# Performance work log

Hardware: AMD Instinct MI355X
Metric: run time of the kernel (lower is better)

## Reference

```python
import jax, jax.numpy as jnp
import numpy as np

B, N, E, F, D = 8, 2000, 64000, 1024, 128
NEG_SLOPE = 0.01  # torch LeakyReLU default

def leaky(x):
    return jnp.where(x >= 0, x, NEG_SLOPE * x)

def gcn_conv(x, ei, W, b):
    # PyG GCNConv: add self loops, symmetric norm, x @ W, scatter-sum, + bias
    src, tgt = ei[0], ei[1]
    loops = jnp.arange(N, dtype=src.dtype)
    src_a = jnp.concatenate([src, loops])
    tgt_a = jnp.concatenate([tgt, loops])
    deg = jax.ops.segment_sum(jnp.ones(src_a.shape, x.dtype), tgt_a, num_segments=N)
    dinv = jnp.where(deg > 0, jax.lax.rsqrt(deg), 0.0)
    norm = dinv[src_a] * dinv[tgt_a]  # [E+N]
    h = x @ W                          # [N, F]
    out = jax.ops.segment_sum(norm[:, None] * h[src_a], tgt_a, num_segments=N)
    return out + b

gcn_conv_b = jax.vmap(gcn_conv, in_axes=(0, 0, None, None))

def setup_inputs() -> dict:
    key = jax.random.key(0)
    ks = jax.random.split(key, 16)
    s = lambda fan: 1.0 / np.sqrt(fan)
    return {
        "x1": jax.random.normal(ks[0], (B, N, F), jnp.float32),
        "ei1": jax.random.randint(ks[1], (B, 2, E), 0, N, jnp.int32),
        "x2": jax.random.normal(ks[2], (B, N, F), jnp.float32),
        "ei2": jax.random.randint(ks[3], (B, 2, E), 0, N, jnp.int32),
        "Wg1": jax.random.normal(ks[4], (F, F), jnp.float32) * s(F),
        "bg1": jnp.zeros((F,), jnp.float32),
        "Wf1": jax.random.normal(ks[5], (F, D), jnp.float32) * s(F),
        "bf1": jnp.zeros((D,), jnp.float32),
        "Wg2": jax.random.normal(ks[6], (F, F), jnp.float32) * s(F),
        "bg2": jnp.zeros((F,), jnp.float32),
        "Wf2": jax.random.normal(ks[7], (F, D), jnp.float32) * s(F),
        "bf2": jnp.zeros((D,), jnp.float32),
        "W1": jax.random.normal(ks[8], (2 * D, 256), jnp.float32) * s(2 * D),
        "b1": jnp.zeros((256,), jnp.float32),
        "W2": jax.random.normal(ks[9], (256, 64), jnp.float32) * s(256),
        "b2": jnp.zeros((64,), jnp.float32),
        "Wo": jax.random.normal(ks[10], (64, 1), jnp.float32) * s(64),
        "bo": jnp.zeros((1,), jnp.float32),
    }

def reference(x1, ei1, x2, ei2, Wg1, bg1, Wf1, bf1, Wg2, bg2, Wf2, bf2,
              W1, b1, W2, b2, Wo, bo):
    # branch 1
    h1 = leaky(gcn_conv_b(x1, ei1, Wg1, bg1))       # [B, N, F]
    g1 = jnp.mean(h1, axis=1)                        # [B, F]
    g1 = leaky(g1 @ Wf1 + bf1)                       # [B, D] (dropout = eval identity)
    # branch 2
    h2 = leaky(gcn_conv_b(x2, ei2, Wg2, bg2))
    g2 = jnp.mean(h2, axis=1)
    g2 = leaky(g2 @ Wf2 + bf2)
    # head
    xc = jnp.concatenate([g1, g2], axis=1)           # [B, 2D]
    xc = leaky(xc @ W1 + b1)
    xc = leaky(xc @ W2 + b2)
    return jax.nn.sigmoid(xc @ Wo + bo)              # [B, 1]
```

## Files before the change

### kernel.cpp

```cpp
#include <hip/hip_runtime.h>
#include <stdint.h>

#define B 8
#define NN 2000
#define EG 64000
#define FF 1024
#define DD 128
#define BK 32
#define NCHUNK 125
#define CG 5

#define NB_CONV 32000
#define NB_WT   2048
#define NB_DEG  4000
#define NB_GEMM 2048
#define NB_FILL 4000

typedef short short8 __attribute__((ext_vector_type(8)));
typedef float f32x4 __attribute__((ext_vector_type(4)));
typedef float f32x2 __attribute__((ext_vector_type(2)));

__device__ __forceinline__ unsigned short f2bf(float f) {
    union { float f; unsigned int u; } v; v.f = f;
    unsigned int u = v.u;
    unsigned int r = u + 0x7FFFu + ((u >> 16) & 1u);
    return (unsigned short)(r >> 16);
}
__device__ __forceinline__ float leaky(float v) { return v >= 0.0f ? v : 0.01f * v; }

__device__ __forceinline__ void acc8p(f32x2* __restrict__ r, float w, uint4 v) {
    union { unsigned int u; float f; } c;
    f32x2 wv = {w, w};
    f32x2 h;
    c.u = v.x << 16;          h.x = c.f;
    c.u = v.x & 0xffff0000u;  h.y = c.f;
    r[0] += wv * h;
    c.u = v.y << 16;          h.x = c.f;
    c.u = v.y & 0xffff0000u;  h.y = c.f;
    r[1] += wv * h;
    c.u = v.z << 16;          h.x = c.f;
    c.u = v.z & 0xffff0000u;  h.y = c.f;
    r[2] += wv * h;
    c.u = v.w << 16;          h.x = c.f;
    c.u = v.w & 0xffff0000u;  h.y = c.f;
    r[3] += wv * h;
}

__global__ void k_prep(const float* __restrict__ x_a, const float* __restrict__ x_b,
                       unsigned short* __restrict__ xb,
                       const float* __restrict__ Wg_a, const float* __restrict__ Wg_b,
                       unsigned short* __restrict__ wT,
                       const int* __restrict__ ei_a, const int* __restrict__ ei_b,
                       int* __restrict__ degi) {
    int blk = blockIdx.x;
    int tid = threadIdx.x;
    __shared__ float tile[32][33];
    if (blk < NB_CONV) {
        int i = blk * 256 + tid;
        float4 v = (i < NB_CONV * 128) ? ((const float4*)x_a)[i]
                                       : ((const float4*)x_b)[i - NB_CONV * 128];
        ushort4 o;
        o.x = f2bf(v.x); o.y = f2bf(v.y); o.z = f2bf(v.z); o.w = f2bf(v.w);
        ((ushort4*)xb)[i] = o;
    } else if (blk < NB_CONV + NB_WT) {
        int b2 = blk - NB_CONV;
        int z = b2 >> 10, rem = b2 & 1023;
        int by = rem >> 5, bx = rem & 31;
        int tx = tid & 31, ty = tid >> 5;
        int k0 = by * 32, n0 = bx * 32;
        const float* Wg = z ? Wg_b : Wg_a;
        unsigned short* o = wT + (size_t)z * FF * FF;
#pragma unroll
        for (int r = 0; r < 4; ++r) {
            int row = ty + r * 8;
            tile[row][tx] = Wg[(k0 + row) * FF + n0 + tx];
        }
        __syncthreads();
#pragma unroll
        for (int r = 0; r < 4; ++r) {
            int row = ty + r * 8;
            o[(n0 + row) * FF + k0 + tx] = f2bf(tile[tx][row]);
        }
    } else {
        int i = (blk - NB_CONV - NB_WT) * 256 + tid;
        int g = i / EG, e = i - g * EG;
        const int* ei = (g < B) ? (ei_a + (size_t)g * 2 * EG)
                                : (ei_b + (size_t)(g - B) * 2 * EG);
        int t = ei[EG + e];
        atomicAdd(&degi[g * NN + t], 1);
    }
}

__global__ void k_scan(const int* __restrict__ degi, int* __restrict__ csr_off,
                       int* __restrict__ cursor, float* __restrict__ dinv) {
    int g = blockIdx.x, t = threadIdx.x;
    __shared__ int part[256];
    int loc[8];
    int s = 0;
#pragma unroll
    for (int i = 0; i < 8; ++i) {
        int n = t * 8 + i;
        int c = (n < NN) ? degi[g * NN + n] : 0;
        if (n < NN) dinv[g * NN + n] = rsqrtf((float)(c + 1));
        loc[i] = s;
        s += c;
    }
    part[t] = s;
    __syncthreads();
    for (int off = 1; off < 256; off <<= 1) {
        int v = (t >= off) ? part[t - off] : 0;
        __syncthreads();
        part[t] += v;
        __syncthreads();
    }
    int base = part[t] - s;
#pragma unroll
    for (int i = 0; i < 8; ++i) {
        int n = t * 8 + i;
        if (n < NN) {
            int o = base + loc[i];
            csr_off[g * (NN + 1) + n] = o;
            cursor[g * NN + n] = o;
        }
    }
    if (t == 255) csr_off[g * (NN + 1) + NN] = part[255];
}

__launch_bounds__(256) __global__
void k_gemm_fill(const unsigned short* __restrict__ Abf, const unsigned short* __restrict__ wT,
                 unsigned short* __restrict__ Hbf,
                 const int* __restrict__ ei_a, const int* __restrict__ ei_b,
                 int* __restrict__ cursor, const float* __restrict__ dinv,
                 int2* __restrict__ epk) {
    int blk = blockIdx.x;
    __shared__ __align__(16) unsigned short As[128 * BK];
    __shared__ __align__(16) unsigned short Bs[128 * BK];
    if (blk >= NB_GEMM) {
        int i = (blk - NB_GEMM) * 256 + threadIdx.x;
        int g = i / EG, e = i - g * EG;
        const int* ei = (g < B) ? (ei_a + (size_t)g * 2 * EG)
                                : (ei_b + (size_t)(g - B) * 2 * EG);
        int s = ei[e];
        int t = ei[EG + e];
        int pos = atomicAdd(&cursor[g * NN + t], 1);
        int2 p;
        p.x = s;
        p.y = __float_as_int(dinv[g * NN + s] * dinv[g * NN + t]);
        epk[(size_t)g * EG + pos] = p;
        return;
    }
    int mt = ((blk >> 6) << 3) | (blk & 7);
    int nt = (blk >> 3) & 7;
    if (mt >= 250) return;
    int m0 = mt * 128, n0 = nt * 128;
    const unsigned short* Bbf = (mt >= 125) ? (wT + (size_t)FF * FF) : wT;

    int tid = threadIdx.x;
    int lane = tid & 63, wave = tid >> 6;
    int wr = wave >> 1, wc = wave & 1;
    int q = lane >> 4, l15 = lane & 15;
    int lr = lane >> 2, lc = lane & 3;

    f32x4 acc[4][4];
#pragma unroll
    for (int i = 0; i < 4; ++i)
#pragma unroll
        for (int j = 0; j < 4; ++j) acc[i][j] = (f32x4){0.f, 0.f, 0.f, 0.f};

    for (int kt = 0; kt < 32; ++kt) {
        int kb = kt * BK;
#pragma unroll
        for (int p = 0; p < 2; ++p) {
            int rbase = p * 64 + wave * 16;
            int r = rbase + lr;
            __builtin_amdgcn_global_load_lds(
                (const __attribute__((address_space(1))) unsigned int*)
                    &Abf[(size_t)(m0 + r) * FF + kb + lc * 8],
                (__attribute__((address_space(3))) unsigned int*)&As[rbase * BK],
                16, 0, 0);
            __builtin_amdgcn_global_load_lds(
                (const __attribute__((address_space(1))) unsigned int*)
                    &Bbf[(size_t)(n0 + r) * FF + kb + lc * 8],
                (__attribute__((address_space(3))) unsigned int*)&Bs[rbase * BK],
                16, 0, 0);
        }
        __syncthreads();
        short8 fa[4], fb[4];
#pragma unroll
        for (int i = 0; i < 4; ++i)
            fa[i] = *(const short8*)&As[(wr * 64 + i * 16 + l15) * BK + q * 8];
#pragma unroll
        for (int j = 0; j < 4; ++j)
            fb[j] = *(const short8*)&Bs[(wc * 64 + j * 16 + l15) * BK + q * 8];
#pragma unroll
        for (int i = 0; i < 4; ++i)
#pragma unroll
            for (int j = 0; j < 4; ++j)
                acc[i][j] = __builtin_amdgcn_mfma_f32_16x16x32_bf16(fa[i], fb[j], acc[i][j], 0, 0, 0);
        __syncthreads();
    }
#pragma unroll
    for (int i = 0; i < 4; ++i) {
#pragma unroll
        for (int j = 0; j < 4; ++j) {
            int n = n0 + wc * 64 + j * 16 + l15;
#pragma unroll
            for (int v = 0; v < 4; ++v) {
                int m = m0 + wr * 64 + i * 16 + q * 4 + v;
                Hbf[(size_t)m * FF + n] = f2bf(acc[i][j][v]);
            }
        }
    }
}

__launch_bounds__(256) __global__
void k_aggreduce(const unsigned short* __restrict__ Hbf, const int* __restrict__ csr_off,
                 const int2* __restrict__ epk, const float* __restrict__ dinv,
                 const float* __restrict__ bg_a, const float* __restrict__ bg_b,
                 float* __restrict__ part) {
    int blk = blockIdx.x;
    int phase = blk / 1000;
    int bp = blk - phase * 1000;
    int half = phase & 1;
    int g = (phase >> 1) * 8 + (bp & 7);
    int chunk = bp >> 3;
    int tid = threadIdx.x;
    int team = tid >> 6;
    int lane = tid & 63;
    int f0 = half * 512 + lane * 8;
    int n0 = chunk * 16 + team * 4;
    const unsigned short* Hb = Hbf + (size_t)g * NN * FF;
    const int2* ep = epk + (size_t)g * EG;
    const float* bg = (g < B) ? bg_a : bg_b;

    f32x2 bgv[4];
#pragma unroll
    for (int i = 0; i < 4; ++i) bgv[i] = (f32x2){bg[f0 + 2 * i], bg[f0 + 2 * i + 1]};
    f32x2 bsum[4];
#pragma unroll
    for (int i = 0; i < 4; ++i) bsum[i] = (f32x2){0.f, 0.f};

    for (int nn = 0; nn < 4; ++nn) {
        int n = n0 + nn;
        float dn = dinv[g * NN + n];
        int beg = csr_off[g * (NN + 1) + n];
        int end = csr_off[g * (NN + 1) + n + 1];
        f32x2 racc[4];
#pragma unroll
        for (int i = 0; i < 4; ++i) racc[i] = (f32x2){0.f, 0.f};
        {
            uint4 sv = *(const uint4*)&Hb[(n << 10) + f0];
            acc8p(racc, dn * dn, sv);
        }
        int j = beg;
        int2 pe0, pe1, pe2, pe3;
        if (j + 4 <= end) { pe0 = ep[j]; pe1 = ep[j + 1]; pe2 = ep[j + 2]; pe3 = ep[j + 3]; }
        for (; j + 8 <= end; j += 4) {
            int2 e0 = pe0, e1 = pe1, e2 = pe2, e3 = pe3;
            pe0 = ep[j + 4]; pe1 = ep[j + 5]; pe2 = ep[j + 6]; pe3 = ep[j + 7];
            uint4 v0 = *(const uint4*)&Hb[(e0.x << 10) + f0];
            uint4 v1 = *(const uint4*)&Hb[(e1.x << 10) + f0];
            uint4 v2 = *(const uint4*)&Hb[(e2.x << 10) + f0];
            uint4 v3 = *(const uint4*)&Hb[(e3.x << 10) + f0];
            acc8p(racc, __int_as_float(e0.y), v0);
            acc8p(racc, __int_as_float(e1.y), v1);
            acc8p(racc, __int_as_float(e2.y), v2);
            acc8p(racc, __int_as_float(e3.y), v3);
        }
        if (j + 4 <= end) {
            uint4 v0 = *(const uint4*)&Hb[(pe0.x << 10) + f0];
            uint4 v1 = *(const uint4*)&Hb[(pe1.x << 10) + f0];
            uint4 v2 = *(const uint4*)&Hb[(pe2.x << 10) + f0];
            uint4 v3 = *(const uint4*)&Hb[(pe3.x << 10) + f0];
            acc8p(racc, __int_as_float(pe0.y), v0);
            acc8p(racc, __int_as_float(pe1.y), v1);
            acc8p(racc, __int_as_float(pe2.y), v2);
            acc8p(racc, __int_as_float(pe3.y), v3);
            j += 4;
        }
        for (; j < end; ++j) {
            int2 e = ep[j];
            uint4 v = *(const uint4*)&Hb[(e.x << 10) + f0];
            acc8p(racc, __int_as_float(e.y), v);
        }
#pragma unroll
        for (int i = 0; i < 4; ++i) {
            f32x2 t = racc[i] + bgv[i];
            bsum[i].x += leaky(t.x);
            bsum[i].y += leaky(t.y);
        }
    }

    __shared__ float red[3][64 * 9];
    if (team > 0) {
#pragma unroll
        for (int i = 0; i < 4; ++i) {
            red[team - 1][lane * 9 + 2 * i]     = bsum[i].x;
            red[team - 1][lane * 9 + 2 * i + 1] = bsum[i].y;
        }
    }
    __syncthreads();
    if (team == 0) {
        float* o = part + ((size_t)g * NCHUNK + chunk) * FF + f0;
        float r[8];
#pragma unroll
        for (int i = 0; i < 4; ++i) {
            r[2 * i]     = bsum[i].x;
            r[2 * i + 1] = bsum[i].y;
        }
#pragma unroll
        for (int t = 0; t < 3; ++t)
#pragma unroll
            for (int i = 0; i < 8; ++i) r[i] += red[t][lane * 9 + i];
        float4 a = {r[0], r[1], r[2], r[3]};
        float4 c = {r[4], r[5], r[6], r[7]};
        *(float4*)&o[0] = a;
        *(float4*)&o[4] = c;
    }
}

__global__ void k_gsum1(const float* __restrict__ part, float* __restrict__ part2) {
    int blk = blockIdx.x;
    int g = blk / 20;
    int rem = blk - g * 20;
    int fq = rem / CG, cg = rem - fq * CG;
    int f = fq * 256 + threadIdx.x;
    const float* p = part + (size_t)g * NCHUNK * FF + (size_t)cg * 25 * FF + f;
    float s = 0.f;
#pragma unroll 5
    for (int c = 0; c < 25; ++c) s += p[(size_t)c * FF];
    part2[((size_t)g * CG + cg) * FF + f] = s;
}

__launch_bounds__(512) __global__
void k_fc(const float* __restrict__ part2, const float* __restrict__ Wf_a,
          const float* __restrict__ bf_a, const float* __restrict__ Wf_b,
          const float* __restrict__ bf_b, float* __restrict__ g12) {
    int g = blockIdx.x, t = threadIdx.x;
    int d = t & 127, slice = t >> 7;
    __shared__ float gs[FF];
    __shared__ float red[4][DD];
    const float* p = part2 + (size_t)g * CG * FF;
#pragma unroll
    for (int i = 0; i < 2; ++i) {
        int f = i * 512 + t;
        float s = 0.f;
#pragma unroll
        for (int c = 0; c < CG; ++c) s += p[(size_t)c * FF + f];
        gs[f] = s;
    }
    __syncthreads();
    const float* Wf = (g < B) ? Wf_a : Wf_b;
    const float* bfv = (g < B) ? bf_a : bf_b;
    float acc = 0.f;
    int fbase = slice * 256;
#pragma unroll 8
    for (int ff = 0; ff < 256; ++ff) {
        int f = fbase + ff;
        acc += gs[f] * Wf[f * DD + d];
    }
    red[slice][d] = acc;
    __syncthreads();
    if (t < DD) {
        float a = red[0][t] + red[1][t] + red[2][t] + red[3][t];
        a = a * (1.0f / (float)NN) + bfv[t];
        g12[g * DD + t] = leaky(a);
    }
}

__launch_bounds__(256) __global__
void k_head(const float* __restrict__ g, const float* __restrict__ W1, const float* __restrict__ b1,
            const float* __restrict__ W2, const float* __restrict__ b2,
            const float* __restrict__ Wo, const float* __restrict__ bo, float* __restrict__ out) {
    __shared__ float xc[8][256];
    __shared__ float l1[8][256];
    __shared__ float l2[8][64];
    int t = threadIdx.x;
#pragma unroll
    for (int i = 0; i < 8; ++i) {
        int idx = i * 256 + t;
        int b = idx >> 8, j = idx & 255;
        xc[b][j] = (j < DD) ? g[b * DD + j] : g[B * DD + b * DD + (j - DD)];
    }
    __syncthreads();
    {
        int j = t;
        float a[8];
#pragma unroll
        for (int b = 0; b < 8; ++b) a[b] = b1[j];
        for (int k = 0; k < 256; ++k) {
            float w = W1[k * 256 + j];
#pragma unroll
            for (int b = 0; b < 8; ++b) a[b] += xc[b][k] * w;
        }
#pragma unroll
        for (int b = 0; b < 8; ++b) l1[b][j] = leaky(a[b]);
    }
    __syncthreads();
    if (t < 64) {
        int j = t;
        float a[8];
#pragma unroll
        for (int b = 0; b < 8; ++b) a[b] = b2[j];
        for (int k = 0; k < 256; ++k) {
            float w = W2[k * 64 + j];
#pragma unroll
            for (int b = 0; b < 8; ++b) a[b] += l1[b][k] * w;
        }
#pragma unroll
        for (int b = 0; b < 8; ++b) l2[b][j] = leaky(a[b]);
    }
    __syncthreads();
    if (t < 8) {
        float a = bo[0];
        for (int k = 0; k < 64; ++k) a += l2[t][k] * Wo[k];
        out[t] = 1.0f / (1.0f + expf(-a));
    }
}

extern "C" void kernel_launch(void* const* d_in, const int* in_sizes, int n_in,
                              void* d_out, int out_size, void* d_ws, size_t ws_size,
                              hipStream_t stream) {
    const float* x1  = (const float*)d_in[0];
    const int*   ei1 = (const int*)d_in[1];
    const float* x2  = (const float*)d_in[2];
    const int*   ei2 = (const int*)d_in[3];
    const float* Wg1 = (const float*)d_in[4];
    const float* bg1 = (const float*)d_in[5];
    const float* Wf1 = (const float*)d_in[6];
    const float* bf1 = (const float*)d_in[7];
    const float* Wg2 = (const float*)d_in[8];
    const float* bg2 = (const float*)d_in[9];
    const float* Wf2 = (const float*)d_in[10];
    const float* bf2 = (const float*)d_in[11];
    const float* W1  = (const float*)d_in[12];
    const float* b1  = (const float*)d_in[13];
    const float* W2  = (const float*)d_in[14];
    const float* b2  = (const float*)d_in[15];
    const float* Wo  = (const float*)d_in[16];
    const float* bo  = (const float*)d_in[17];
    float* out = (float*)d_out;

    auto align = [](size_t v) { return (v + 255) & ~(size_t)255; };
    size_t need = 0;
    size_t o_deg  = need; need += align((size_t)16 * NN * 4);
    size_t o_dinv = need; need += align((size_t)16 * NN * 4);
    size_t o_csr  = need; need += align((size_t)16 * (NN + 1) * 4);
    size_t o_cur  = need; need += align((size_t)16 * NN * 4);
    size_t o_epk  = need; need += align((size_t)16 * EG * 8);
    size_t o_xbf  = need; need += align((size_t)16 * NN * FF * 2);
    size_t o_wT   = need; need += align((size_t)2 * FF * FF * 2);
    size_t o_hbf  = need; need += align((size_t)16 * NN * FF * 2);
    size_t o_part = need; need += align((size_t)16 * NCHUNK * FF * 4);
    size_t o_pt2  = need; need += align((size_t)16 * CG * FF * 4);
    size_t o_g12  = need; need += align((size_t)16 * DD * 4);
    (void)need;

    char* w = (char*)d_ws;
    int* degi    = (int*)(w + o_deg);
    float* dinv  = (float*)(w + o_dinv);
    int* csr     = (int*)(w + o_csr);
    int* cur     = (int*)(w + o_cur);
    int2* epk    = (int2*)(w + o_epk);
    unsigned short* xbf = (unsigned short*)(w + o_xbf);
    unsigned short* wT  = (unsigned short*)(w + o_wT);
    unsigned short* hbf = (unsigned short*)(w + o_hbf);
    float* part  = (float*)(w + o_part);
    float* part2 = (float*)(w + o_pt2);
    float* g12   = (float*)(w + o_g12);

    hipMemsetAsync(degi, 0, (size_t)16 * NN * 4, stream);
    k_prep<<<NB_CONV + NB_WT + NB_DEG, 256, 0, stream>>>(x1, x2, xbf, Wg1, Wg2, wT,
                                                         ei1, ei2, degi);
    k_scan<<<16, 256, 0, stream>>>(degi, csr, cur, dinv);
    k_gemm_fill<<<NB_GEMM + NB_FILL, 256, 0, stream>>>(xbf, wT, hbf, ei1, ei2, cur,
                                                       dinv, epk);
    k_aggreduce<<<4000, 256, 0, stream>>>(hbf, csr, epk, dinv, bg1, bg2, part);
    k_gsum1<<<16 * 20, 256, 0, stream>>>(part, part2);
    k_fc<<<16, 512, 0, stream>>>(part2, Wf1, bf1, Wf2, bf2, g12);
    k_head<<<1, 256, 0, stream>>>(g12, W1, b1, W2, b2, Wo, bo, out);
}
```

Measured before the change: 529.5 us.

## Rewrite bf16 GEMM with 256x256 tiles, double-buffered LDS, and fused edge fill

Replaces the 128x128 GEMM tile kernel with a 512-thread kernel that computes 256x256 tiles over a K step of 64. The LDS is double-buffered (128KB), loaded with swizzled direct global-to-LDS copies, and the loads of the next K slice are interleaved with MFMA phases under explicit barriers and priority hints. The CSR edge fill now runs at the tail of each GEMM block instead of in separate blocks. This aims for more operand reuse and better overlap of loads with MFMA work. The cost is fewer blocks (504) with a partial last M tile that needs padding in the x buffer, and a serialized fill step after each block's GEMM.

```diff
diff --git a/kernel.cpp b/kernel.cpp
--- a/kernel.cpp
+++ b/kernel.cpp
@@ -13,8 +13,8 @@
 #define NB_CONV 32000
 #define NB_WT   2048
 #define NB_DEG  4000
-#define NB_GEMM 2048
-#define NB_FILL 4000
+#define NTK 16
+#define NB_G8 504
 
 typedef short short8 __attribute__((ext_vector_type(8)));
 typedef float f32x4 __attribute__((ext_vector_type(4)));
@@ -126,89 +126,161 @@
     if (t == 255) csr_off[g * (NN + 1) + NN] = part[255];
 }
 
-__launch_bounds__(256) __global__
-void k_gemm_fill(const unsigned short* __restrict__ Abf, const unsigned short* __restrict__ wT,
-                 unsigned short* __restrict__ Hbf,
-                 const int* __restrict__ ei_a, const int* __restrict__ ei_b,
-                 int* __restrict__ cursor, const float* __restrict__ dinv,
-                 int2* __restrict__ epk) {
-    int blk = blockIdx.x;
-    __shared__ __align__(16) unsigned short As[128 * BK];
-    __shared__ __align__(16) unsigned short Bs[128 * BK];
-    if (blk >= NB_GEMM) {
-        int i = (blk - NB_GEMM) * 256 + threadIdx.x;
-        int g = i / EG, e = i - g * EG;
-        const int* ei = (g < B) ? (ei_a + (size_t)g * 2 * EG)
-                                : (ei_b + (size_t)(g - B) * 2 * EG);
-        int s = ei[e];
-        int t = ei[EG + e];
-        int pos = atomicAdd(&cursor[g * NN + t], 1);
-        int2 p;
-        p.x = s;
-        p.y = __float_as_int(dinv[g * NN + s] * dinv[g * NN + t]);
-        epk[(size_t)g * EG + pos] = p;
-        return;
-    }
-    int mt = ((blk >> 6) << 3) | (blk & 7);
-    int nt = (blk >> 3) & 7;
-    if (mt >= 250) return;
-    int m0 = mt * 128, n0 = nt * 128;
-    const unsigned short* Bbf = (mt >= 125) ? (wT + (size_t)FF * FF) : wT;
+__launch_bounds__(512, 2) __global__
+void k_gemm8(const unsigned short* __restrict__ Abf, const unsigned short* __restrict__ wT,
+             unsigned short* __restrict__ Hbf,
+             const int* __restrict__ ei_a, const int* __restrict__ ei_b,
+             int* __restrict__ cursor, const float* __restrict__ dinv,
+             int2* __restrict__ epk) {
+    __shared__ __align__(16) char smem[131072];
+    int bid = blockIdx.x;
+    int wg = (bid & 7) * 63 + (bid >> 3);
+    int mt = wg >> 2, nt = wg & 3;
+    int set = (mt >= 63) ? 1 : 0;
+    int m0 = set * 16000 + (mt - set * 63) * 256;
+    int n0 = nt * 256;
+    int mlim = set * 16000 + 16000;
+    const unsigned short* Bg = wT + (size_t)set * FF * FF;
 
     int tid = threadIdx.x;
     int lane = tid & 63, wave = tid >> 6;
-    int wr = wave >> 1, wc = wave & 1;
-    int q = lane >> 4, l15 = lane & 15;
-    int lr = lane >> 2, lc = lane & 3;
-
-    f32x4 acc[4][4];
-#pragma unroll
-    for (int i = 0; i < 4; ++i)
+    int wr = wave >> 2, wc = wave & 3;
+    int l15 = lane & 15, q = lane >> 4;
+    int qx = q ^ (((l15 >> 2) & 1) << 1);
+    int arow = wr * 128 + l15;
+    int brow = wc * 64 + l15;
+    int col8s = (tid & 7) ^ (((tid >> 5) & 1) << 1);
+    int srow = tid >> 3;
+    unsigned wbase = (unsigned)wave << 10;
+
+    f32x4 acc[8][4];
+#pragma unroll
+    for (int i = 0; i < 8; ++i)
 #pragma unroll
         for (int j = 0; j < 4; ++j) acc[i][j] = (f32x4){0.f, 0.f, 0.f, 0.f};
 
-    for (int kt = 0; kt < 32; ++kt) {
-        int kb = kt * BK;
-#pragma unroll
-        for (int p = 0; p < 2; ++p) {
-            int rbase = p * 64 + wave * 16;
-            int r = rbase + lr;
-            __builtin_amdgcn_global_load_lds(
-                (const __attribute__((address_space(1))) unsigned int*)
-                    &Abf[(size_t)(m0 + r) * FF + kb + lc * 8],
-                (__attribute__((address_space(3))) unsigned int*)&As[rbase * BK],
-                16, 0, 0);
-            __builtin_amdgcn_global_load_lds(
-                (const __attribute__((address_space(1))) unsigned int*)
-                    &Bbf[(size_t)(n0 + r) * FF + kb + lc * 8],
-                (__attribute__((address_space(3))) unsigned int*)&Bs[rbase * BK],
-                16, 0, 0);
-        }
-        __syncthreads();
+    auto stage = [&](int ktn, int isB, int hh) {
+        const unsigned short* gsrc = isB ? Bg : Abf;
+        int x0 = isB ? n0 : m0;
+        int r1 = x0 + hh * 128 + srow;
+        int kb = ktn * 64 + col8s * 8;
+        unsigned db = ((unsigned)(ktn & 1) << 16) | ((unsigned)isB << 15)
+                    | ((unsigned)hh << 14) | wbase;
+        __builtin_amdgcn_global_load_lds(
+            (const __attribute__((address_space(1))) unsigned int*)(gsrc + (size_t)r1 * FF + kb),
+            (__attribute__((address_space(3))) unsigned int*)&smem[db], 16, 0, 0);
+        __builtin_amdgcn_global_load_lds(
+            (const __attribute__((address_space(1))) unsigned int*)(gsrc + (size_t)(r1 + 64) * FF + kb),
+            (__attribute__((address_space(3))) unsigned int*)&smem[db + 8192], 16, 0, 0);
+    };
+
+    stage(0, 0, 0); stage(0, 0, 1); stage(0, 1, 0); stage(0, 1, 1);
+
+    unsigned bb = 0;
+    auto lda = [&](int i, int kk) -> short8 {
+        return *(const short8*)&smem[bb + ((unsigned)(arow + i * 16) << 7)
+                                        + ((unsigned)(kk * 4 + qx) << 4)];
+    };
+    auto ldb = [&](int j, int kk) -> short8 {
+        return *(const short8*)&smem[bb + 32768u + ((unsigned)(brow + j * 16) << 7)
+                                        + ((unsigned)(kk * 4 + qx) << 4)];
+    };
+
+    for (int kt = 0; kt < NTK; ++kt) {
+        asm volatile("s_waitcnt vmcnt(0)" ::: "memory");
+        __builtin_amdgcn_s_barrier();
+        bb = (unsigned)(kt & 1) << 16;
         short8 fa[4], fb[4];
 #pragma unroll
-        for (int i = 0; i < 4; ++i)
-            fa[i] = *(const short8*)&As[(wr * 64 + i * 16 + l15) * BK + q * 8];
-#pragma unroll
-        for (int j = 0; j < 4; ++j)
-            fb[j] = *(const short8*)&Bs[(wc * 64 + j * 16 + l15) * BK + q * 8];
+        for (int j = 0; j < 4; ++j) fb[j] = ldb(j, 0);
+#pragma unroll
+        for (int i = 0; i < 4; ++i) fa[i] = lda(i, 0);
+        if (kt + 1 < NTK) stage(kt + 1, 0, 0);
+        __builtin_amdgcn_s_barrier();
+        asm volatile("s_waitcnt lgkmcnt(0)" ::: "memory");
+        __builtin_amdgcn_sched_barrier(0);
+        __builtin_amdgcn_s_setprio(1);
 #pragma unroll
         for (int i = 0; i < 4; ++i)
 #pragma unroll
             for (int j = 0; j < 4; ++j)
                 acc[i][j] = __builtin_amdgcn_mfma_f32_16x16x32_bf16(fa[i], fb[j], acc[i][j], 0, 0, 0);
-        __syncthreads();
-    }
-#pragma unroll
-    for (int i = 0; i < 4; ++i) {
+        __builtin_amdgcn_s_setprio(0);
+        __builtin_amdgcn_s_barrier();
+#pragma unroll
+        for (int i = 0; i < 4; ++i) fa[i] = lda(i + 4, 0);
+        if (kt + 1 < NTK) stage(kt + 1, 0, 1);
+        __builtin_amdgcn_s_barrier();
+        asm volatile("s_waitcnt lgkmcnt(0)" ::: "memory");
+        __builtin_amdgcn_sched_barrier(0);
+        __builtin_amdgcn_s_setprio(1);
+#pragma unroll
+        for (int i = 0; i < 4; ++i)
+#pragma unroll
+            for (int j = 0; j < 4; ++j)
+                acc[i + 4][j] = __builtin_amdgcn_mfma_f32_16x16x32_bf16(fa[i], fb[j], acc[i + 4][j], 0, 0, 0);
+        __builtin_amdgcn_s_setprio(0);
+        __builtin_amdgcn_s_barrier();
+#pragma unroll
+        for (int j = 0; j < 4; ++j) fb[j] = ldb(j, 1);
+#pragma unroll
+        for (int i = 0; i < 4; ++i) fa[i] = lda(i, 1);
+        if (kt + 1 < NTK) stage(kt + 1, 1, 0);
+        __builtin_amdgcn_s_barrier();
+        asm volatile("s_waitcnt lgkmcnt(0)" ::: "memory");
+        __builtin_amdgcn_sched_barrier(0);
+        __builtin_amdgcn_s_setprio(1);
+#pragma unroll
+        for (int i = 0; i < 4; ++i)
+#pragma unroll
+            for (int j = 0; j < 4; ++j)
+                acc[i][j] = __builtin_amdgcn_mfma_f32_16x16x32_bf16(fa[i], fb[j], acc[i][j], 0, 0, 0);
+        __builtin_amdgcn_s_setprio(0);
+        __builtin_amdgcn_s_barrier();
+#pragma unroll
+        for (int i = 0; i < 4; ++i) fa[i] = lda(i + 4, 1);
+        if (kt + 1 < NTK) stage(kt + 1, 1, 1);
+        __builtin_amdgcn_s_barrier();
+        asm volatile("s_waitcnt lgkmcnt(0)" ::: "memory");
+        __builtin_amdgcn_sched_barrier(0);
+        __builtin_amdgcn_s_setprio(1);
+#pragma unroll
+        for (int i = 0; i < 4; ++i)
+#pragma unroll
+            for (int j = 0; j < 4; ++j)
+                acc[i + 4][j] = __builtin_amdgcn_mfma_f32_16x16x32_bf16(fa[i], fb[j], acc[i + 4][j], 0, 0, 0);
+        __builtin_amdgcn_s_setprio(0);
+        __builtin_amdgcn_s_barrier();
+    }
+
+#pragma unroll
+    for (int i = 0; i < 8; ++i) {
 #pragma unroll
         for (int j = 0; j < 4; ++j) {
             int n = n0 + wc * 64 + j * 16 + l15;
 #pragma unroll
             for (int v = 0; v < 4; ++v) {
-                int m = m0 + wr * 64 + i * 16 + q * 4 + v;
-                Hbf[(size_t)m * FF + n] = f2bf(acc[i][j][v]);
+                int m = m0 + wr * 128 + i * 16 + q * 4 + v;
+                if (m < mlim) Hbf[(size_t)m * FF + n] = f2bf(acc[i][j][v]);
             }
+        }
+    }
+
+    int ebase = bid * 512 + tid;
+#pragma unroll
+    for (int r = 0; r < 4; ++r) {
+        int idx = ebase + r * (NB_G8 * 512);
+        if (idx < 16 * EG) {
+            int gg = idx / EG, e = idx - gg * EG;
+            const int* ei = (gg < B) ? (ei_a + (size_t)gg * 2 * EG)
+                                     : (ei_b + (size_t)(gg - B) * 2 * EG);
+            int s = ei[e];
+            int t = ei[EG + e];
+            int pos = atomicAdd(&cursor[gg * NN + t], 1);
+            int2 p;
+            p.x = s;
+            p.y = __float_as_int(dinv[gg * NN + s] * dinv[gg * NN + t]);
+            epk[(size_t)gg * EG + pos] = p;
         }
     }
 }
@@ -448,7 +520,7 @@
     size_t o_csr  = need; need += align((size_t)16 * (NN + 1) * 4);
     size_t o_cur  = need; need += align((size_t)16 * NN * 4);
     size_t o_epk  = need; need += align((size_t)16 * EG * 8);
-    size_t o_xbf  = need; need += align((size_t)16 * NN * FF * 2);
+    size_t o_xbf  = need; need += align(((size_t)16 * NN + 128) * FF * 2);
     size_t o_wT   = need; need += align((size_t)2 * FF * FF * 2);
     size_t o_hbf  = need; need += align((size_t)16 * NN * FF * 2);
     size_t o_part = need; need += align((size_t)16 * NCHUNK * FF * 4);
@@ -473,8 +545,7 @@
     k_prep<<<NB_CONV + NB_WT + NB_DEG, 256, 0, stream>>>(x1, x2, xbf, Wg1, Wg2, wT,
                                                          ei1, ei2, degi);
     k_scan<<<16, 256, 0, stream>>>(degi, csr, cur, dinv);
-    k_gemm_fill<<<NB_GEMM + NB_FILL, 256, 0, stream>>>(xbf, wT, hbf, ei1, ei2, cur,
-                                                       dinv, epk);
+    k_gemm8<<<NB_G8, 512, 0, stream>>>(xbf, wT, hbf, ei1, ei2, cur, dinv, epk);
     k_aggreduce<<<4000, 256, 0, stream>>>(hbf, csr, epk, dinv, bg1, bg2, part);
     k_gsum1<<<16 * 20, 256, 0, stream>>>(part, part2);
     k_fc<<<16, 512, 0, stream>>>(part2, Wf1, bf1, Wf2, bf2, g12);
```

Measured after the change: 544.0 us. 1.03x slower.
